# Kernel optimization log

Measured on AMD Instinct MI355X. Metric: run time of the kernel, lower is better.

## Reference

```python
import jax, jax.numpy as jnp
import numpy as np

B, MAX_S, HID = 128, 4096, 5120
H, D_NOPE, D_ROPE, D_V = 128, 128, 64, 128
KV_SIZE = 512 + 64  # kv_lora_rank + qk_rope_head_dim = 576


def setup_inputs() -> dict:
    key = jax.random.key(0)
    ks = jax.random.split(key, 8)
    seq_lens = jax.random.randint(ks[0], (B,), 1, MAX_S)
    return {
        "hidden_states": jax.random.normal(ks[1], (B, 1, HID), jnp.float32),
        "k_cache": jax.random.normal(ks[2], (B, MAX_S, D_NOPE), jnp.float32),
        "v_cache": jax.random.normal(ks[3], (B, MAX_S, D_V), jnp.float32),
        "Wq": jax.random.normal(ks[4], (HID, H * (D_NOPE + D_ROPE)), jnp.float32) * 0.02,
        "Wkv": jax.random.normal(ks[5], (HID, KV_SIZE), jnp.float32) * 0.02,
        "Wo": jax.random.normal(ks[6], (H * D_V, HID), jnp.float32) * 0.02,
        "positions": seq_lens - 1,
        "slot_mapping": seq_lens - 1,
        "seq_lens": seq_lens,
    }


def reference(hidden_states, k_cache, v_cache, Wq, Wkv, Wo, positions, slot_mapping, seq_lens):
    h = hidden_states[:, -1, :]                        # [B, HID] last-token decode
    q = (h @ Wq).reshape(B, H, D_NOPE + D_ROPE)        # [B, H, 192]
    kv = h @ Wkv                                       # [B, 576]
    q_nope = q[:, :, :D_NOPE]                          # [B, H, 128]
    k_new = kv[:, :D_NOPE]                             # [B, 128]
    v_new = kv[:, D_NOPE:D_NOPE + D_V]                 # [B, 128]

    b_idx = jnp.arange(B)
    kc = k_cache.at[b_idx, slot_mapping].set(k_new)    # write new token into paged cache
    vc = v_cache.at[b_idx, slot_mapping].set(v_new)

    scale = D_NOPE ** -0.5
    scores = jnp.einsum('bhd,bsd->bhs', q_nope, kc) * scale  # MQA: 1 kv head broadcast
    valid = jnp.arange(MAX_S)[None, :] < seq_lens[:, None]   # [B, S]
    scores = jnp.where(valid[:, None, :], scores, jnp.float32(-1e30))
    p = jax.nn.softmax(scores, axis=-1)
    attn = jnp.einsum('bhs,bsd->bhd', p, vc)           # [B, H, 128]

    return attn.reshape(B, 1, H * D_V) @ Wo            # [B, 1, HID]
```

## Files before the change

### kernel.cpp

```cpp
#include <hip/hip_runtime.h>

typedef __attribute__((ext_vector_type(4))) float f32x4;
typedef __attribute__((ext_vector_type(8))) short bf16x8;
typedef __attribute__((ext_vector_type(2))) unsigned int u32x2;
typedef __attribute__((ext_vector_type(4))) unsigned int u32x4;

static __device__ __forceinline__ unsigned short f2bf(float f) {
    unsigned u = __builtin_bit_cast(unsigned, f);
    u += 0x7fffu + ((u >> 16) & 1u);
    return (unsigned short)(u >> 16);
}
static __device__ __forceinline__ unsigned pack2(float a, float b) {
    return (unsigned)f2bf(a) | ((unsigned)f2bf(b) << 16);
}

template<int ABF16, int COLMAP>
__global__ __launch_bounds__(256, 4)
void gemm128(const void* __restrict__ A_, int lda,
             const float* __restrict__ Bm, int ldb,
             float* __restrict__ Cp, int ldc,
             int kchunk, int nsplit)
{
    __shared__ __align__(16) unsigned short As[128 * 72];
    __shared__ __align__(16) unsigned short Bs[64 * 66];

    const int tid = threadIdx.x;
    const int w = tid >> 6, l = tid & 63, lg = l >> 4, l15 = l & 15;
    const int bx = blockIdx.x / nsplit;
    const int by = blockIdx.x % nsplit;
    const int n0 = bx * 64;
    const int pcol = COLMAP ? ((n0 >> 7) * 192 + (n0 & 127)) : n0;
    const size_t k0base = (size_t)by * (size_t)kchunk;
    float* __restrict__ C = Cp + (size_t)by * ((size_t)128 * (size_t)ldc);

    const int ar  = tid >> 3;
    const int ac8 = (tid & 7) * 8;
    const int br  = tid >> 1;
    const int bc  = (tid & 1) * 32;
    const int bnb = (tid & 15) * 4;
    const int bkk = tid >> 4;

    f32x4 aReg[4][2];
    u32x4 aRegH[4];
    f32x4 b0Reg[2][2], b1Reg[2][2];

    const float* Af = (const float*)A_;
    const unsigned short* Ah = (const unsigned short*)A_;

    auto loadA = [&](size_t k0) {
        if (ABF16) {
#pragma unroll
            for (int k = 0; k < 4; k++)
                aRegH[k] = *(const u32x4*)(Ah + (size_t)br * lda + k0 + bc + 8 * k);
        } else {
#pragma unroll
            for (int j = 0; j < 4; j++) {
                const float* p = Af + (size_t)(ar + 32 * j) * lda + k0 + ac8;
                aReg[j][0] = *(const f32x4*)p;
                aReg[j][1] = *(const f32x4*)(p + 4);
            }
        }
    };
    auto storeA = [&]() {
        if (ABF16) {
#pragma unroll
            for (int k = 0; k < 4; k++)
                *(u32x4*)&As[br * 72 + bc + 8 * k] = aRegH[k];
        } else {
#pragma unroll
            for (int j = 0; j < 4; j++) {
                u32x4 wv = { pack2(aReg[j][0][0], aReg[j][0][1]), pack2(aReg[j][0][2], aReg[j][0][3]),
                             pack2(aReg[j][1][0], aReg[j][1][1]), pack2(aReg[j][1][2], aReg[j][1][3]) };
                *(u32x4*)&As[(ar + 32 * j) * 72 + ac8] = wv;
            }
        }
    };
    auto loadB = [&](f32x4 (&bR)[2][2], size_t k0) {
#pragma unroll
        for (int i = 0; i < 2; i++) {
            const float* bp = Bm + (k0 + (size_t)(2 * (bkk + 16 * i))) * (size_t)ldb + pcol + bnb;
            bR[i][0] = *(const f32x4*)bp;
            bR[i][1] = *(const f32x4*)(bp + ldb);
        }
    };
    auto storeB = [&](f32x4 (&bR)[2][2]) {
        unsigned* bd = (unsigned*)Bs;
#pragma unroll
        for (int i = 0; i < 2; i++)
#pragma unroll
            for (int j = 0; j < 4; j++)
                bd[(bnb + j) * 33 + bkk + 16 * i] = pack2(bR[i][0][j], bR[i][1][j]);
    };

    f32x4 acc[2][4];
    const f32x4 fzero = {0.f, 0.f, 0.f, 0.f};
#pragma unroll
    for (int a = 0; a < 2; a++)
#pragma unroll
        for (int b2 = 0; b2 < 4; b2++) acc[a][b2] = fzero;

    auto mfmaStep = [&]() {
#pragma unroll
        for (int ks = 0; ks < 2; ks++) {
            bf16x8 bfr[4];
#pragma unroll
            for (int nf = 0; nf < 4; nf++)
                bfr[nf] = *(const bf16x8*)&Bs[(16 * nf + l15) * 66 + 32 * ks + 8 * lg];
#pragma unroll
            for (int mf = 0; mf < 2; mf++) {
                bf16x8 af = *(const bf16x8*)&As[(32 * w + 16 * mf + l15) * 72 + 32 * ks + 8 * lg];
#pragma unroll
                for (int nf = 0; nf < 4; nf++)
                    acc[mf][nf] = __builtin_amdgcn_mfma_f32_16x16x32_bf16(af, bfr[nf], acc[mf][nf], 0, 0, 0);
            }
        }
    };

    const int nst = kchunk >> 6;
    auto kof = [&](int t) { return k0base + (size_t)(t << 6); };

    loadA(kof(0));
    loadB(b0Reg, kof(0));
    if (nst > 1) loadB(b1Reg, kof(1));

    for (int t = 0; t < nst; t += 2) {
        storeA(); storeB(b0Reg);
        __syncthreads();
        if (t + 1 < nst) loadA(kof(t + 1));
        if (t + 2 < nst) loadB(b0Reg, kof(t + 2));
        __builtin_amdgcn_sched_barrier(0);
        mfmaStep();
        __syncthreads();
        if (t + 1 < nst) {
            storeA(); storeB(b1Reg);
            __syncthreads();
            if (t + 2 < nst) loadA(kof(t + 2));
            if (t + 3 < nst) loadB(b1Reg, kof(t + 3));
            __builtin_amdgcn_sched_barrier(0);
            mfmaStep();
            __syncthreads();
        }
    }
#pragma unroll
    for (int mf = 0; mf < 2; mf++) {
#pragma unroll
        for (int nf = 0; nf < 4; nf++) {
            const int m0 = 32 * w + 16 * mf + 4 * lg;
            const int cn = n0 + 16 * nf + l15;
#pragma unroll
            for (int r = 0; r < 4; r++)
                C[(size_t)(m0 + r) * ldc + cn] = acc[mf][nf][r];
        }
    }
}

__global__ __launch_bounds__(256)
void reduce_f32(const float* __restrict__ in, float* __restrict__ out, int n4, int ns)
{
    const int i = blockIdx.x * 256 + threadIdx.x;
    if (i >= n4) return;
    const f32x4* in4 = (const f32x4*)in;
    f32x4 s = in4[i];
    for (int j = 1; j < ns; j++) s += in4[i + (size_t)j * n4];
    ((f32x4*)out)[i] = s;
}

__global__ __launch_bounds__(256)
void reduce_q_bf16(const float* __restrict__ in, unsigned* __restrict__ out)
{
    const int i = blockIdx.x * 256 + threadIdx.x;
    const f32x4* in4 = (const f32x4*)in;
    f32x4 s = in4[i] + in4[i + 524288] + in4[i + 2 * 524288] + in4[i + 3 * 524288];
    const float scale = 0.088388347648318447f;
    s *= scale;
    u32x2 p = { pack2(s[0], s[1]), pack2(s[2], s[3]) };
    *(u32x2*)&out[2 * i] = p;
}

#define NSPLIT 8
#define CHUNK_T 8

__global__ __launch_bounds__(512, 4)
void attn_fwd(const float* __restrict__ kc, const float* __restrict__ vc,
              const unsigned short* __restrict__ qb, const float* __restrict__ kvp,
              const int* __restrict__ seq_lens, const int* __restrict__ slot_map,
              float* __restrict__ Opart, float* __restrict__ m_ws, float* __restrict__ l_ws)
{
    __shared__ __align__(16) unsigned short Ks [64 * 136];
    __shared__ __align__(16) unsigned short Vts[128 * 72];
    __shared__ __align__(16) unsigned short Ps [128 * 72];
    __shared__ float knew_s[128];
    __shared__ float vnew_s[128];

    const int b = blockIdx.x, split = blockIdx.y;
    const int seq = seq_lens[b], slot = slot_map[b];
    const int nt = (seq + 63) >> 6;
    const int t0 = split * CHUNK_T;
    const int t1 = min(t0 + CHUNK_T, nt);
    const int slotTile = slot >> 6;

    const int tid = threadIdx.x, w = tid >> 6, l = tid & 63, lg = l >> 4, l15 = l & 15;
    const int h = 16 * w + l15;

    float m_run = -__builtin_inff(), l_run = 0.0f;

    if (t0 < t1) {
        if (slotTile >= t0 && slotTile < t1 && tid < 256) {
            float s = 0.f;
#pragma unroll
            for (int j = 0; j < 8; j++) s += kvp[j * 32768 + b * 256 + tid];
            if (tid < 128) knew_s[tid] = s;
            else           vnew_s[tid - 128] = s;
        }

        bf16x8 qf[4];
        {
            const unsigned short* qrow = qb + (size_t)b * 16384 + (size_t)h * 128;
#pragma unroll
            for (int ks = 0; ks < 4; ks++)
                qf[ks] = *(const bf16x8*)(qrow + 32 * ks + 8 * lg);
        }

        f32x4 kReg[4];
        f32x4 vReg[2][2];
        const int kr  = tid >> 3;
        const int kcb = (tid & 7) * 16;
        const int vsp = tid & 31;
        const int vdq = tid >> 5;

        auto loadKV = [&](int t) {
            const int s0 = t << 6;
            const float* ksrc = kc + ((size_t)b * 4096 + s0 + kr) * 128 + kcb;
#pragma unroll
            for (int c = 0; c < 4; c++) kReg[c] = *(const f32x4*)(ksrc + 4 * c);
#pragma unroll
            for (int i = 0; i < 2; i++) {
                const int d4 = 4 * vdq + 64 * i;
                const float* r1 = vc + ((size_t)b * 4096 + s0 + 2 * vsp) * 128 + d4;
                vReg[i][0] = *(const f32x4*)r1;
                vReg[i][1] = *(const f32x4*)(r1 + 128);
            }
        };
        auto storeKV = [&]() {
            u32x4 w0 = { pack2(kReg[0][0], kReg[0][1]), pack2(kReg[0][2], kReg[0][3]),
                         pack2(kReg[1][0], kReg[1][1]), pack2(kReg[1][2], kReg[1][3]) };
            u32x4 w1 = { pack2(kReg[2][0], kReg[2][1]), pack2(kReg[2][2], kReg[2][3]),
                         pack2(kReg[3][0], kReg[3][1]), pack2(kReg[3][2], kReg[3][3]) };
            *(u32x4*)&Ks[kr * 136 + kcb] = w0;
            *(u32x4*)&Ks[kr * 136 + kcb + 8] = w1;
            unsigned* vt = (unsigned*)Vts;
#pragma unroll
            for (int i = 0; i < 2; i++)
#pragma unroll
                for (int j = 0; j < 4; j++)
                    vt[(4 * vdq + 64 * i + j) * 36 + vsp] = pack2(vReg[i][0][j], vReg[i][1][j]);
        };

        f32x4 accO[8];
        const f32x4 fzero = {0.f, 0.f, 0.f, 0.f};
#pragma unroll
        for (int i = 0; i < 8; i++) accO[i] = fzero;

        loadKV(t0);
        for (int t = t0; t < t1; ++t) {
            const int s0 = t << 6;
            storeKV();
            __syncthreads();
            if (t == slotTile) {
                if (tid < 128) {
                    const int sloc = slot & 63;
                    Ks [sloc * 136 + tid] = f2bf(knew_s[tid]);
                    Vts[tid * 72 + sloc]  = f2bf(vnew_s[tid]);
                }
                __syncthreads();
            }
            if (t + 1 < t1) loadKV(t + 1);
            __builtin_amdgcn_sched_barrier(0);

            f32x4 accS[4];
#pragma unroll
            for (int sf = 0; sf < 4; sf++) accS[sf] = fzero;
#pragma unroll
            for (int ks = 0; ks < 4; ks++) {
#pragma unroll
                for (int sf = 0; sf < 4; sf++) {
                    bf16x8 kf = *(const bf16x8*)&Ks[(16 * sf + l15) * 136 + 32 * ks + 8 * lg];
                    accS[sf] = __builtin_amdgcn_mfma_f32_16x16x32_bf16(kf, qf[ks], accS[sf], 0, 0, 0);
                }
            }
            float tmax = -__builtin_inff();
#pragma unroll
            for (int sf = 0; sf < 4; sf++) {
#pragma unroll
                for (int r = 0; r < 4; r++) {
                    const int s = s0 + 16 * sf + 4 * lg + r;
                    float sc = (s < seq) ? accS[sf][r] : -__builtin_inff();
                    accS[sf][r] = sc;
                    tmax = fmaxf(tmax, sc);
                }
            }
            tmax = fmaxf(tmax, __shfl_xor(tmax, 16));
            tmax = fmaxf(tmax, __shfl_xor(tmax, 32));
            const float mnew = fmaxf(m_run, tmax);
            const float so = __expf(m_run - mnew);
            float lsum = 0.f;
#pragma unroll
            for (int sf = 0; sf < 4; sf++) {
#pragma unroll
                for (int r = 0; r < 4; r++) {
                    const float p = __expf(accS[sf][r] - mnew);
                    accS[sf][r] = p;
                    lsum += p;
                }
            }
            lsum += __shfl_xor(lsum, 16);
            lsum += __shfl_xor(lsum, 32);
            l_run = l_run * so + lsum;
            m_run = mnew;
#pragma unroll
            for (int i = 0; i < 8; i++) accO[i] *= so;

            {
                unsigned* pd = (unsigned*)Ps;
#pragma unroll
                for (int sf = 0; sf < 4; sf++) {
                    pd[h * 36 + 8 * sf + 2 * lg + 0] = pack2(accS[sf][0], accS[sf][1]);
                    pd[h * 36 + 8 * sf + 2 * lg + 1] = pack2(accS[sf][2], accS[sf][3]);
                }
            }
            bf16x8 pf[2];
#pragma unroll
            for (int ks = 0; ks < 2; ks++)
                pf[ks] = *(const bf16x8*)&Ps[h * 72 + 32 * ks + 8 * lg];
#pragma unroll
            for (int df = 0; df < 8; df++) {
#pragma unroll
                for (int ks = 0; ks < 2; ks++) {
                    bf16x8 vf = *(const bf16x8*)&Vts[(16 * df + l15) * 72 + 32 * ks + 8 * lg];
                    accO[df] = __builtin_amdgcn_mfma_f32_16x16x32_bf16(vf, pf[ks], accO[df], 0, 0, 0);
                }
            }
            __syncthreads();
        }
        const size_t base = ((size_t)(b * NSPLIT + split)) * 16384 + (size_t)h * 128;
#pragma unroll
        for (int df = 0; df < 8; df++)
            *(f32x4*)&Opart[base + 16 * df + 4 * lg] = accO[df];
    }
    if (lg == 0) {
        m_ws[(b * NSPLIT + split) * 128 + h] = m_run;
        l_ws[(b * NSPLIT + split) * 128 + h] = l_run;
    }
}

__global__ __launch_bounds__(256)
void combine8(const float* __restrict__ Opart, const float* __restrict__ m_ws,
              const float* __restrict__ l_ws, unsigned* __restrict__ attn_bf)
{
    const int idx = blockIdx.x * 256 + threadIdx.x;
    const int d4 = (idx & 31) * 4;
    const int hh = (idx >> 5) & 127;
    const int b = idx >> 12;

    float m = -__builtin_inff();
    float mv[NSPLIT], lv[NSPLIT];
#pragma unroll
    for (int j = 0; j < NSPLIT; j++) {
        mv[j] = m_ws[(b * NSPLIT + j) * 128 + hh];
        lv[j] = l_ws[(b * NSPLIT + j) * 128 + hh];
        m = fmaxf(m, mv[j]);
    }
    f32x4 o = {0.f, 0.f, 0.f, 0.f};
    float lsum = 0.f;
#pragma unroll
    for (int j = 0; j < NSPLIT; j++) {
        const float a = (lv[j] > 0.f) ? __expf(mv[j] - m) : 0.f;
        lsum += a * lv[j];
        if (a > 0.f) {
            f32x4 oj = *(const f32x4*)&Opart[((size_t)(b * NSPLIT + j)) * 16384 + (size_t)hh * 128 + d4];
            o += oj * a;
        }
    }
    o *= (1.0f / lsum);
    u32x2 p = { pack2(o[0], o[1]), pack2(o[2], o[3]) };
    *(u32x2*)&attn_bf[(size_t)b * 8192 + (size_t)hh * 64 + (d4 >> 1)] = p;
}

extern "C" void kernel_launch(void* const* d_in, const int* in_sizes, int n_in,
                              void* d_out, int out_size, void* d_ws, size_t ws_size,
                              hipStream_t stream)
{
    const float* hidden  = (const float*)d_in[0];
    const float* k_cache = (const float*)d_in[1];
    const float* v_cache = (const float*)d_in[2];
    const float* Wq      = (const float*)d_in[3];
    const float* Wkv     = (const float*)d_in[4];
    const float* Wo      = (const float*)d_in[5];
    const int* slot_map  = (const int*)d_in[7];
    const int* seq_lens  = (const int*)d_in[8];
    float* out = (float*)d_out;

    float* ws      = (float*)d_ws;
    float* qp      = ws;
    float* qb      = ws + 8388608;
    float* kvp     = ws + 9437184;
    float* attn_bf = ws + 9699328;
    float* Opart   = ws + 10747904;
    float* m_ws    = ws + 27525120;
    float* l_ws    = ws + 27656192;
    float* outp    = ws + 27787264;

    gemm128<0, 0><<<dim3(4 * 8), 256, 0, stream>>>(hidden, 5120, Wkv, 576, kvp, 256, 640, 8);
    gemm128<0, 1><<<dim3(256 * 4), 256, 0, stream>>>(hidden, 5120, Wq, 24576, qp, 16384, 1280, 4);
    reduce_q_bf16<<<dim3(2048), 256, 0, stream>>>(qp, (unsigned*)qb);
    attn_fwd<<<dim3(128, NSPLIT), 512, 0, stream>>>(k_cache, v_cache, (const unsigned short*)qb,
                                                    kvp, seq_lens, slot_map, Opart, m_ws, l_ws);
    combine8<<<dim3(2048), 256, 0, stream>>>(Opart, m_ws, l_ws, (unsigned*)attn_bf);
    gemm128<1, 0><<<dim3(80 * 8), 256, 0, stream>>>(attn_bf, 16384, Wo, 5120, outp, 5120, 2048, 8);
    reduce_f32<<<dim3(640), 256, 0, stream>>>(outp, out, 163840, 8);
}
```

Measured before the change: 369.2 us.

## Pre-convert hidden to bf16, use non-draining barriers, and raise split-K for small GEMMs

Adds a kernel that converts hidden states to bf16 once, so the Wq and Wkv GEMMs load half as much A data and skip repeated conversion. __syncthreads is replaced by a barrier that waits only on LDS operations, so prefetched global loads stay in flight across the barrier. The Wkv and Wo GEMMs go from 8-way to 16-way split-K for more parallelism. pack2 now uses the HIP bf16 intrinsic. The extra kernel launch and a larger partial-sum reduction are the added costs, and the non-draining barrier depends on the LDS stores being complete before other threads read them.

```diff
diff --git a/kernel.cpp b/kernel.cpp
--- a/kernel.cpp
+++ b/kernel.cpp
@@ -1,4 +1,5 @@
 #include <hip/hip_runtime.h>
+#include <hip/hip_bf16.h>
 
 typedef __attribute__((ext_vector_type(4))) float f32x4;
 typedef __attribute__((ext_vector_type(8))) short bf16x8;
@@ -11,12 +12,33 @@
     return (unsigned short)(u >> 16);
 }
 static __device__ __forceinline__ unsigned pack2(float a, float b) {
-    return (unsigned)f2bf(a) | ((unsigned)f2bf(b) << 16);
-}
-
-template<int ABF16, int COLMAP>
+    __hip_bfloat162 h = __float22bfloat162_rn(make_float2(a, b));
+    unsigned u;
+    __builtin_memcpy(&u, &h, 4);
+    return u;
+}
+
+static __device__ __forceinline__ void bar_nodrain() {
+    __builtin_amdgcn_sched_barrier(0);
+    asm volatile("s_waitcnt lgkmcnt(0)" ::: "memory");
+    __builtin_amdgcn_s_barrier();
+    __builtin_amdgcn_sched_barrier(0);
+}
+
+__global__ __launch_bounds__(256)
+void cvt_bf16(const float* __restrict__ in, unsigned* __restrict__ out, int n8)
+{
+    const int i = blockIdx.x * 256 + threadIdx.x;
+    if (i >= n8) return;
+    f32x4 a = ((const f32x4*)in)[2 * i];
+    f32x4 b = ((const f32x4*)in)[2 * i + 1];
+    u32x4 p = { pack2(a[0], a[1]), pack2(a[2], a[3]), pack2(b[0], b[1]), pack2(b[2], b[3]) };
+    ((u32x4*)out)[i] = p;
+}
+
+template<int COLMAP>
 __global__ __launch_bounds__(256, 4)
-void gemm128(const void* __restrict__ A_, int lda,
+void gemm128(const unsigned short* __restrict__ Ah, int lda,
              const float* __restrict__ Bm, int ldb,
              float* __restrict__ Cp, int ldc,
              int kchunk, int nsplit)
@@ -33,47 +55,23 @@
     const size_t k0base = (size_t)by * (size_t)kchunk;
     float* __restrict__ C = Cp + (size_t)by * ((size_t)128 * (size_t)ldc);
 
-    const int ar  = tid >> 3;
-    const int ac8 = (tid & 7) * 8;
-    const int br  = tid >> 1;
-    const int bc  = (tid & 1) * 32;
+    const int ar = tid >> 1;
+    const int ac = (tid & 1) * 32;
     const int bnb = (tid & 15) * 4;
     const int bkk = tid >> 4;
 
-    f32x4 aReg[4][2];
-    u32x4 aRegH[4];
+    u32x4 aReg[4];
     f32x4 b0Reg[2][2], b1Reg[2][2];
 
-    const float* Af = (const float*)A_;
-    const unsigned short* Ah = (const unsigned short*)A_;
-
     auto loadA = [&](size_t k0) {
-        if (ABF16) {
-#pragma unroll
-            for (int k = 0; k < 4; k++)
-                aRegH[k] = *(const u32x4*)(Ah + (size_t)br * lda + k0 + bc + 8 * k);
-        } else {
-#pragma unroll
-            for (int j = 0; j < 4; j++) {
-                const float* p = Af + (size_t)(ar + 32 * j) * lda + k0 + ac8;
-                aReg[j][0] = *(const f32x4*)p;
-                aReg[j][1] = *(const f32x4*)(p + 4);
-            }
-        }
+#pragma unroll
+        for (int k = 0; k < 4; k++)
+            aReg[k] = *(const u32x4*)(Ah + (size_t)ar * lda + k0 + ac + 8 * k);
     };
     auto storeA = [&]() {
-        if (ABF16) {
-#pragma unroll
-            for (int k = 0; k < 4; k++)
-                *(u32x4*)&As[br * 72 + bc + 8 * k] = aRegH[k];
-        } else {
-#pragma unroll
-            for (int j = 0; j < 4; j++) {
-                u32x4 wv = { pack2(aReg[j][0][0], aReg[j][0][1]), pack2(aReg[j][0][2], aReg[j][0][3]),
-                             pack2(aReg[j][1][0], aReg[j][1][1]), pack2(aReg[j][1][2], aReg[j][1][3]) };
-                *(u32x4*)&As[(ar + 32 * j) * 72 + ac8] = wv;
-            }
-        }
+#pragma unroll
+        for (int k = 0; k < 4; k++)
+            *(u32x4*)&As[ar * 72 + ac + 8 * k] = aReg[k];
     };
     auto loadB = [&](f32x4 (&bR)[2][2], size_t k0) {
 #pragma unroll
@@ -125,20 +123,20 @@
 
     for (int t = 0; t < nst; t += 2) {
         storeA(); storeB(b0Reg);
-        __syncthreads();
+        bar_nodrain();
         if (t + 1 < nst) loadA(kof(t + 1));
         if (t + 2 < nst) loadB(b0Reg, kof(t + 2));
         __builtin_amdgcn_sched_barrier(0);
         mfmaStep();
-        __syncthreads();
+        bar_nodrain();
         if (t + 1 < nst) {
             storeA(); storeB(b1Reg);
-            __syncthreads();
+            bar_nodrain();
             if (t + 2 < nst) loadA(kof(t + 2));
             if (t + 3 < nst) loadB(b1Reg, kof(t + 3));
             __builtin_amdgcn_sched_barrier(0);
             mfmaStep();
-            __syncthreads();
+            bar_nodrain();
         }
     }
 #pragma unroll
@@ -179,6 +177,7 @@
 
 #define NSPLIT 8
 #define CHUNK_T 8
+#define KVSPLIT 16
 
 __global__ __launch_bounds__(512, 4)
 void attn_fwd(const float* __restrict__ kc, const float* __restrict__ vc,
@@ -208,7 +207,7 @@
         if (slotTile >= t0 && slotTile < t1 && tid < 256) {
             float s = 0.f;
 #pragma unroll
-            for (int j = 0; j < 8; j++) s += kvp[j * 32768 + b * 256 + tid];
+            for (int j = 0; j < KVSPLIT; j++) s += kvp[j * 32768 + b * 256 + tid];
             if (tid < 128) knew_s[tid] = s;
             else           vnew_s[tid - 128] = s;
         }
@@ -265,14 +264,14 @@
         for (int t = t0; t < t1; ++t) {
             const int s0 = t << 6;
             storeKV();
-            __syncthreads();
+            bar_nodrain();
             if (t == slotTile) {
                 if (tid < 128) {
                     const int sloc = slot & 63;
                     Ks [sloc * 136 + tid] = f2bf(knew_s[tid]);
                     Vts[tid * 72 + sloc]  = f2bf(vnew_s[tid]);
                 }
-                __syncthreads();
+                bar_nodrain();
             }
             if (t + 1 < t1) loadKV(t + 1);
             __builtin_amdgcn_sched_barrier(0);
@@ -340,7 +339,7 @@
                     accO[df] = __builtin_amdgcn_mfma_f32_16x16x32_bf16(vf, pf[ks], accO[df], 0, 0, 0);
                 }
             }
-            __syncthreads();
+            bar_nodrain();
         }
         const size_t base = ((size_t)(b * NSPLIT + split)) * 16384 + (size_t)h * 128;
 #pragma unroll
@@ -401,21 +400,23 @@
     float* out = (float*)d_out;
 
     float* ws      = (float*)d_ws;
-    float* qp      = ws;
-    float* qb      = ws + 8388608;
-    float* kvp     = ws + 9437184;
-    float* attn_bf = ws + 9699328;
-    float* Opart   = ws + 10747904;
-    float* m_ws    = ws + 27525120;
-    float* l_ws    = ws + 27656192;
-    float* outp    = ws + 27787264;
-
-    gemm128<0, 0><<<dim3(4 * 8), 256, 0, stream>>>(hidden, 5120, Wkv, 576, kvp, 256, 640, 8);
-    gemm128<0, 1><<<dim3(256 * 4), 256, 0, stream>>>(hidden, 5120, Wq, 24576, qp, 16384, 1280, 4);
+    float* hb      = ws;
+    float* qp      = ws + 327680;
+    float* qb      = ws + 8716288;
+    float* kvp     = ws + 9764864;
+    float* attn_bf = ws + 10289152;
+    float* Opart   = ws + 11337728;
+    float* m_ws    = ws + 28114944;
+    float* l_ws    = ws + 28246016;
+    float* outp    = ws + 28377088;
+
+    cvt_bf16<<<dim3(320), 256, 0, stream>>>(hidden, (unsigned*)hb, 81920);
+    gemm128<0><<<dim3(4 * 16), 256, 0, stream>>>((const unsigned short*)hb, 5120, Wkv, 576, kvp, 256, 320, 16);
+    gemm128<1><<<dim3(256 * 4), 256, 0, stream>>>((const unsigned short*)hb, 5120, Wq, 24576, qp, 16384, 1280, 4);
     reduce_q_bf16<<<dim3(2048), 256, 0, stream>>>(qp, (unsigned*)qb);
     attn_fwd<<<dim3(128, NSPLIT), 512, 0, stream>>>(k_cache, v_cache, (const unsigned short*)qb,
                                                     kvp, seq_lens, slot_map, Opart, m_ws, l_ws);
     combine8<<<dim3(2048), 256, 0, stream>>>(Opart, m_ws, l_ws, (unsigned*)attn_bf);
-    gemm128<1, 0><<<dim3(80 * 8), 256, 0, stream>>>(attn_bf, 16384, Wo, 5120, outp, 5120, 2048, 8);
-    reduce_f32<<<dim3(640), 256, 0, stream>>>(outp, out, 163840, 8);
-}
+    gemm128<0><<<dim3(80 * 16), 256, 0, stream>>>((const unsigned short*)attn_bf, 16384, Wo, 5120, outp, 5120, 1024, 16);
+    reduce_f32<<<dim3(640), 256, 0, stream>>>(outp, out, 163840, 16);
+}
```

Result: faster. 322.1 us (-12.8%).
